# Kernel tuning notes

Measured on AMD Instinct MI355X. Metric: run time of the kernel, lower is better.

Reference implementation:

```python
import jax, jax.numpy as jnp
import numpy as np

N, E, IN, H, L, NB, G = 50000, 300000, 64, 256, 4, 181, 64
EPS = 1e-5
NEG_SLOPE = 0.2


def segment_softmax(e, seg, n):
    m = jax.ops.segment_max(e, seg, num_segments=n)
    a = jnp.exp(e - m[seg])
    d = jax.ops.segment_sum(a, seg, num_segments=n)
    return a / d[seg]


def setup_inputs() -> dict:
    key = jax.random.key(0)
    ks = jax.random.split(key, 32)
    p = lambda k, shape, fan: (jax.random.normal(k, shape, jnp.float32) / np.sqrt(fan)).astype(jnp.float32)
    inp = {}
    inp["x"] = jax.random.normal(ks[0], (N, IN), jnp.float32)
    inp["edge_index"] = jax.random.randint(ks[1], (2, E), 0, N, jnp.int64)
    inp["batch"] = jnp.sort(jax.random.randint(ks[2], (N,), 0, G, jnp.int64))
    inp["W_in"] = p(ks[3], (H, IN), IN); inp["b_in"] = jnp.zeros((H,), jnp.float32)
    inp["Wl"] = p(ks[4], (L, H, H), H); inp["bl"] = jnp.zeros((L, H), jnp.float32)
    inp["Wr"] = p(ks[5], (L, H, H), H); inp["br"] = jnp.zeros((L, H), jnp.float32)
    inp["att"] = p(ks[6], (L, H), H)
    inp["bias_c"] = jnp.zeros((L, H), jnp.float32)
    inp["ln_g"] = jnp.ones((L, H), jnp.float32); inp["ln_b"] = jnp.zeros((L, H), jnp.float32)
    inp["Wg1"] = p(ks[7], (H, H), H); inp["bg1"] = jnp.zeros((H,), jnp.float32)
    inp["Wg2"] = p(ks[8], (1, H), H); inp["bg2"] = jnp.zeros((1,), jnp.float32)
    inp["Ws"] = p(ks[9], (H, H), H); inp["bs"] = jnp.zeros((H,), jnp.float32)
    inp["Wc"] = p(ks[10], (NB, H), H); inp["bc"] = jnp.zeros((NB,), jnp.float32)
    inp["Wr1"] = p(ks[11], (128, H), H); inp["br1"] = jnp.zeros((128,), jnp.float32)
    inp["Wr2"] = p(ks[12], (1, 128), 128); inp["br2"] = jnp.zeros((1,), jnp.float32)
    return inp


def reference(x, edge_index, batch, W_in, b_in, Wl, bl, Wr, br, att, bias_c, ln_g, ln_b,
              Wg1, bg1, Wg2, bg2, Ws, bs, Wc, bc, Wr1, br1, Wr2, br2):
    n = x.shape[0]
    x = x @ W_in.T + b_in  # input projection -> [N,H]
    loops = jnp.arange(n)
    src = jnp.concatenate([edge_index[0], loops])  # GATv2 add_self_loops=True
    dst = jnp.concatenate([edge_index[1], loops])
    for l in range(L):
        x_res = x
        xl = x @ Wl[l].T + bl[l]  # lin_l (source)
        xr = x @ Wr[l].T + br[l]  # lin_r (target)
        h = jax.nn.leaky_relu(xl[src] + xr[dst], NEG_SLOPE)  # [E+N, H]
        e = h @ att[l]                                       # [E+N]
        alpha = segment_softmax(e, dst, n)
        out = jax.ops.segment_sum(alpha[:, None] * xl[src], dst, num_segments=n) + bias_c[l]
        mu = out.mean(-1, keepdims=True)
        var = out.var(-1, keepdims=True)
        out = (out - mu) / jnp.sqrt(var + EPS) * ln_g[l] + ln_b[l]
        x = jax.nn.relu(out) + x_res  # dropout is identity at eval
    gate = jax.nn.relu(x @ Wg1.T + bg1) @ Wg2.T + bg2  # [N,1]
    a = segment_softmax(gate[:, 0], batch, G)
    pooled = jax.ops.segment_sum(a[:, None] * x, batch, num_segments=G)  # [G,H]
    z = jax.nn.relu(pooled @ Ws.T + bs)
    cls_logits = z @ Wc.T + bc                                   # [G,NB]
    residual = jnp.tanh(jax.nn.relu(z @ Wr1.T + br1) @ Wr2.T + br2)[:, 0]  # [G]
    return cls_logits, residual
```

## Files before the change

kernel.cpp:

```cpp
#include <hip/hip_runtime.h>
#include <math.h>

#define N_NODES 50000
#define N_EDGES 300000
#define IN_DIM 64
#define H 256
#define LAYERS 4
#define NB 181
#define NGRAPH 64
#define EE (N_EDGES + N_NODES)
#define NEG_SLOPE 0.2f
#define LN_EPS 1e-5f

typedef unsigned short u16;
typedef __attribute__((ext_vector_type(8))) _Float16 half8;
typedef __attribute__((ext_vector_type(2))) _Float16 half2v;
typedef __attribute__((ext_vector_type(4))) float floatx4;

__device__ __forceinline__ u16 f2h(float f) {
  _Float16 h = (_Float16)f;
  return __builtin_bit_cast(u16, h);
}
__device__ __forceinline__ float h2f(u16 b) {
  return (float)__builtin_bit_cast(_Float16, b);
}

__device__ __forceinline__ float wave_reduce_sum(float v) {
  #pragma unroll
  for (int off = 32; off > 0; off >>= 1) v += __shfl_xor(v, off, 64);
  return v;
}

__global__ void cast_f16_kernel(const float* __restrict__ in, u16* __restrict__ out, int n4) {
  int i = blockIdx.x * 256 + threadIdx.x;
  if (i < n4) {
    float4 f = ((const float4*)in)[i];
    ushort4 o;
    o.x = f2h(f.x); o.y = f2h(f.y); o.z = f2h(f.z); o.w = f2h(f.w);
    ((ushort4*)out)[i] = o;
  }
}

__global__ void cast_weights_kernel(
    const float* __restrict__ W_in, const float* __restrict__ Wg1,
    const float* __restrict__ Wl, const float* __restrict__ Wr,
    u16* __restrict__ win_h, u16* __restrict__ wg1_h,
    u16* __restrict__ wl_h, u16* __restrict__ wr_h)
{
  int i = blockIdx.x * 256 + threadIdx.x;
  int which = blockIdx.y;
  const float* s; u16* dd; int n4;
  if (which == 0)      { s = W_in; dd = win_h; n4 = H * IN_DIM / 4; }
  else if (which == 1) { s = Wg1;  dd = wg1_h; n4 = H * H / 4; }
  else if (which == 2) { s = Wl;   dd = wl_h;  n4 = LAYERS * H * H / 4; }
  else                 { s = Wr;   dd = wr_h;  n4 = LAYERS * H * H / 4; }
  if (i < n4) {
    float4 f = ((const float4*)s)[i];
    ushort4 o;
    o.x = f2h(f.x); o.y = f2h(f.y); o.z = f2h(f.z); o.w = f2h(f.w);
    ((ushort4*)dd)[i] = o;
  }
}

__global__ void init_counts_kernel(int* __restrict__ cnt) {
  int i = blockIdx.x * 256 + threadIdx.x;
  if (i < N_NODES) cnt[i] = 1;
}

__global__ void count_edges_kernel(const int* __restrict__ dst, int* __restrict__ cnt) {
  int e = blockIdx.x * 256 + threadIdx.x;
  if (e < N_EDGES) atomicAdd(&cnt[dst[e]], 1);
}

__global__ void scan_blocks_kernel(const int* __restrict__ cnt, int* __restrict__ partial,
                                   int* __restrict__ bsums, int n) {
  __shared__ int buf[256];
  int tid = threadIdx.x;
  int i = blockIdx.x * 256 + tid;
  buf[tid] = (i < n) ? cnt[i] : 0;
  __syncthreads();
  #pragma unroll
  for (int off = 1; off < 256; off <<= 1) {
    int t = (tid >= off) ? buf[tid - off] : 0;
    __syncthreads();
    buf[tid] += t;
    __syncthreads();
  }
  if (i < n) partial[i] = buf[tid];
  if (tid == 255) bsums[blockIdx.x] = buf[255];
}

__global__ void scan_sums_kernel(int* __restrict__ bsums, int nblk) {
  __shared__ int buf[256];
  int tid = threadIdx.x;
  buf[tid] = (tid < nblk) ? bsums[tid] : 0;
  __syncthreads();
  #pragma unroll
  for (int off = 1; off < 256; off <<= 1) {
    int t = (tid >= off) ? buf[tid - off] : 0;
    __syncthreads();
    buf[tid] += t;
    __syncthreads();
  }
  if (tid < nblk) bsums[tid] = buf[tid];
}

__global__ void scan_write_kernel(const int* __restrict__ partial, const int* __restrict__ bsums,
                                  int* __restrict__ rowp, int n) {
  int i = blockIdx.x * 256 + threadIdx.x;
  if (i < n) {
    int b = blockIdx.x;
    int off = (b > 0) ? bsums[b - 1] : 0;
    rowp[i + 1] = partial[i] + off;
    if (i == 0) rowp[0] = 0;
  }
}

__global__ void fill_self_kernel(const int* __restrict__ rowp, int* __restrict__ col,
                                 int* __restrict__ fillpos) {
  int i = blockIdx.x * 256 + threadIdx.x;
  if (i < N_NODES) {
    int p = rowp[i];
    col[p] = i;
    fillpos[i] = p + 1;
  }
}

__global__ void fill_edges_kernel(const int* __restrict__ src, const int* __restrict__ dst,
                                  int* __restrict__ fillpos, int* __restrict__ col) {
  int e = blockIdx.x * 256 + threadIdx.x;
  if (e < N_EDGES) {
    int d = dst[e];
    int p = atomicAdd(&fillpos[d], 1);
    col[p] = src[e];
  }
}

#define GTM 128
#define GTK 64
#define LDB 72
#define SSTR 132

__global__ __launch_bounds__(256) void gemm_proj_kernel(
    const u16* __restrict__ A, const u16* __restrict__ W,
    const float* __restrict__ bias, u16* __restrict__ outh, int M, int K)
{
  __shared__ u16 smem[2 * GTM * LDB];
  u16* As = smem;
  u16* Bs = smem + GTM * LDB;
  int tid = threadIdx.x;
  int lane = tid & 63;
  int wave = tid >> 6;
  int wm = (wave >> 1) * 64;
  int wn = (wave & 1) * 64;
  int bm = blockIdx.y * GTM;
  int n0 = blockIdx.x * 128;
  int lr = tid >> 3;
  int lc = (tid & 7) * 8;

  floatx4 zero4 = {0.f, 0.f, 0.f, 0.f};
  floatx4 acc[4][4];
  #pragma unroll
  for (int i = 0; i < 4; i++)
    #pragma unroll
    for (int j = 0; j < 4; j++) acc[i][j] = zero4;

  int q8 = (lane >> 4) * 8;
  int mrow = lane & 15;

  for (int k0 = 0; k0 < K; k0 += GTK) {
    __syncthreads();
    #pragma unroll
    for (int p = 0; p < 4; p++) {
      int row = lr + p * 32;
      int gr = bm + row;
      uint4 av = {0, 0, 0, 0};
      if (gr < M) av = *(const uint4*)&A[(size_t)gr * K + k0 + lc];
      *(uint4*)&As[row * LDB + lc] = av;
      uint4 bv = *(const uint4*)&W[(size_t)(n0 + row) * K + k0 + lc];
      *(uint4*)&Bs[row * LDB + lc] = bv;
    }
    __syncthreads();
    #pragma unroll
    for (int h = 0; h < 2; h++) {
      half8 af[4], bf[4];
      #pragma unroll
      for (int i = 0; i < 4; i++)
        af[i] = *(const half8*)&As[(wm + i * 16 + mrow) * LDB + h * 32 + q8];
      #pragma unroll
      for (int j = 0; j < 4; j++)
        bf[j] = *(const half8*)&Bs[(wn + j * 16 + mrow) * LDB + h * 32 + q8];
      #pragma unroll
      for (int i = 0; i < 4; i++)
        #pragma unroll
        for (int j = 0; j < 4; j++)
          acc[i][j] = __builtin_amdgcn_mfma_f32_16x16x32_f16(af[i], bf[j], acc[i][j], 0, 0, 0);
    }
  }

  __syncthreads();
  u16* stage = smem;
  int ccol = lane & 15;
  int crow4 = (lane >> 4) * 4;
  #pragma unroll
  for (int j = 0; j < 4; j++) {
    float bv = bias[n0 + wn + j * 16 + ccol];
    #pragma unroll
    for (int i = 0; i < 4; i++) {
      #pragma unroll
      for (int r = 0; r < 4; r++) {
        int row = wm + i * 16 + crow4 + r;
        stage[row * SSTR + wn + j * 16 + ccol] = f2h(acc[i][j][r] + bv);
      }
    }
  }
  __syncthreads();
  int rr = tid >> 1;
  int c0 = (tid & 1) * 64;
  int grow = bm + rr;
  if (grow < M) {
    const ushort4* sp = (const ushort4*)&stage[rr * SSTR + c0];
    ushort4* gp = (ushort4*)&outh[(size_t)grow * H + n0 + c0];
    #pragma unroll
    for (int q = 0; q < 16; q++) gp[q] = sp[q];
  }
}

#define DTM 64
#define AST 264
#define SSTR2 132

__global__ __launch_bounds__(256) void gemm_dual2_kernel(
    const u16* __restrict__ A, const u16* __restrict__ Wlb, const u16* __restrict__ Wrb,
    const float* __restrict__ biasL, const float* __restrict__ biasR,
    u16* __restrict__ outL, u16* __restrict__ outR, int M)
{
  __shared__ u16 As[DTM * AST];
  __shared__ u16 Bs[128 * LDB];
  int tid = threadIdx.x;
  int lane = tid & 63;
  int wave = tid >> 6;
  int wn = wave * 32;
  int bm = blockIdx.x * DTM;
  int mrow = lane & 15;
  int q8 = (lane >> 4) * 8;
  int ccol = lane & 15;
  int crow4 = (lane >> 4) * 4;

  {
    int col = (tid & 31) * 8;
    int r0 = tid >> 5;
    #pragma unroll
    for (int it = 0; it < 8; it++) {
      int row = r0 + it * 8;
      int gr = bm + row;
      uint4 av = {0, 0, 0, 0};
      if (gr < M) av = *(const uint4*)&A[(size_t)gr * H + col];
      *(uint4*)&As[row * AST + col] = av;
    }
  }

  floatx4 zero4 = {0.f, 0.f, 0.f, 0.f};

  for (int nt = 0; nt < 4; nt++) {
    const u16* W = (nt < 2) ? Wlb : Wrb;
    const float* bias = (nt < 2) ? biasL : biasR;
    u16* outp = (nt < 2) ? outL : outR;
    int n0 = (nt & 1) * 128;

    floatx4 acc[4][2];
    #pragma unroll
    for (int i = 0; i < 4; i++) {
      acc[i][0] = zero4;
      acc[i][1] = zero4;
    }

    for (int k0 = 0; k0 < H; k0 += 64) {
      __syncthreads();
      {
        int col = (tid & 7) * 8;
        int r0 = tid >> 3;
        #pragma unroll
        for (int p2 = 0; p2 < 4; p2++) {
          int row = r0 + p2 * 32;
          uint4 bv = *(const uint4*)&W[(size_t)(n0 + row) * H + k0 + col];
          *(uint4*)&Bs[row * LDB + col] = bv;
        }
      }
      __syncthreads();
      #pragma unroll
      for (int h = 0; h < 2; h++) {
        half8 af[4], bf[2];
        #pragma unroll
        for (int i = 0; i < 4; i++)
          af[i] = *(const half8*)&As[(i * 16 + mrow) * AST + k0 + h * 32 + q8];
        #pragma unroll
        for (int j = 0; j < 2; j++)
          bf[j] = *(const half8*)&Bs[(wn + j * 16 + mrow) * LDB + h * 32 + q8];
        #pragma unroll
        for (int i = 0; i < 4; i++)
          #pragma unroll
          for (int j = 0; j < 2; j++)
            acc[i][j] = __builtin_amdgcn_mfma_f32_16x16x32_f16(af[i], bf[j], acc[i][j], 0, 0, 0);
      }
    }

    __syncthreads();
    u16* stage = Bs;
    #pragma unroll
    for (int j = 0; j < 2; j++) {
      float bv = bias[n0 + wn + j * 16 + ccol];
      #pragma unroll
      for (int i = 0; i < 4; i++) {
        #pragma unroll
        for (int r = 0; r < 4; r++) {
          int row = i * 16 + crow4 + r;
          stage[row * SSTR2 + wn + j * 16 + ccol] = f2h(acc[i][j][r] + bv);
        }
      }
    }
    __syncthreads();
    {
      int row = tid >> 2;
      int c0 = (tid & 3) * 32;
      int grow = bm + row;
      if (grow < M) {
        #pragma unroll
        for (int q = 0; q < 8; q++)
          *(ushort4*)&outp[(size_t)grow * H + n0 + c0 + q * 4] =
              *(const ushort4*)&stage[row * SSTR2 + c0 + q * 4];
      }
    }
  }
}

__global__ __launch_bounds__(256) void gemm_gate_kernel(
    const u16* __restrict__ A, const u16* __restrict__ W,
    const float* __restrict__ bias, const float* __restrict__ Wg2,
    float* __restrict__ gate, int M)
{
  __shared__ u16 smem[2 * GTM * LDB];
  u16* As = smem;
  u16* Bs = smem + GTM * LDB;
  int tid = threadIdx.x;
  int lane = tid & 63;
  int wave = tid >> 6;
  int wm = (wave >> 1) * 64;
  int wn = (wave & 1) * 64;
  int bm = blockIdx.y * GTM;
  int bn = blockIdx.x * 128;
  int lr = tid >> 3;
  int lc = (tid & 7) * 8;

  floatx4 zero4 = {0.f, 0.f, 0.f, 0.f};
  floatx4 acc[4][4];
  #pragma unroll
  for (int i = 0; i < 4; i++)
    #pragma unroll
    for (int j = 0; j < 4; j++) acc[i][j] = zero4;

  int q8 = (lane >> 4) * 8;
  int mrow = lane & 15;

  for (int k0 = 0; k0 < H; k0 += GTK) {
    __syncthreads();
    #pragma unroll
    for (int p = 0; p < 4; p++) {
      int row = lr + p * 32;
      int gr = bm + row;
      uint4 av = {0, 0, 0, 0};
      if (gr < M) av = *(const uint4*)&A[(size_t)gr * H + k0 + lc];
      *(uint4*)&As[row * LDB + lc] = av;
      uint4 bv = *(const uint4*)&W[(size_t)(bn + row) * H + k0 + lc];
      *(uint4*)&Bs[row * LDB + lc] = bv;
    }
    __syncthreads();
    #pragma unroll
    for (int h = 0; h < 2; h++) {
      half8 af[4], bf[4];
      #pragma unroll
      for (int i = 0; i < 4; i++)
        af[i] = *(const half8*)&As[(wm + i * 16 + mrow) * LDB + h * 32 + q8];
      #pragma unroll
      for (int j = 0; j < 4; j++)
        bf[j] = *(const half8*)&Bs[(wn + j * 16 + mrow) * LDB + h * 32 + q8];
      #pragma unroll
      for (int i = 0; i < 4; i++)
        #pragma unroll
        for (int j = 0; j < 4; j++)
          acc[i][j] = __builtin_amdgcn_mfma_f32_16x16x32_f16(af[i], bf[j], acc[i][j], 0, 0, 0);
    }
  }

  int ccol = lane & 15;
  float bv[4], wv[4];
  #pragma unroll
  for (int j = 0; j < 4; j++) {
    int col = bn + wn + j * 16 + ccol;
    bv[j] = bias[col];
    wv[j] = Wg2[col];
  }
  #pragma unroll
  for (int i = 0; i < 4; i++) {
    #pragma unroll
    for (int r = 0; r < 4; r++) {
      float p = 0.f;
      #pragma unroll
      for (int j = 0; j < 4; j++) {
        float hcol = fmaxf(acc[i][j][r] + bv[j], 0.f);
        p += hcol * wv[j];
      }
      p += __shfl_xor(p, 1, 64);
      p += __shfl_xor(p, 2, 64);
      p += __shfl_xor(p, 4, 64);
      p += __shfl_xor(p, 8, 64);
      int row = bm + wm + i * 16 + (lane >> 4) * 4 + r;
      if ((lane & 15) == 0 && row < M) atomicAdd(&gate[row], p);
    }
  }
}

__global__ __launch_bounds__(256) void layer_fused_kernel(
    const u16* __restrict__ xl, const u16* __restrict__ xr,
    u16* __restrict__ xst,
    const int* __restrict__ rowp, const int* __restrict__ col,
    const float* __restrict__ att, const float* __restrict__ bias_c,
    const float* __restrict__ ln_g, const float* __restrict__ ln_b)
{
  int lane = threadIdx.x & 63;
  int v = blockIdx.x * 4 + (threadIdx.x >> 6);
  if (v >= N_NODES) return;
  int slot = lane >> 5;
  int fl = lane & 31;
  int f8 = fl << 3;
  size_t rowbase = (size_t)v * H;

  uint4 xrq = *(const uint4*)&xr[rowbase + f8];
  half2v xrh[4] = {
    __builtin_bit_cast(half2v, xrq.x), __builtin_bit_cast(half2v, xrq.y),
    __builtin_bit_cast(half2v, xrq.z), __builtin_bit_cast(half2v, xrq.w)};
  float4 attA = *(const float4*)&att[f8];
  float4 attB = *(const float4*)&att[f8 + 4];
  half2v ath[4] = {
    {(_Float16)attA.x, (_Float16)attA.y}, {(_Float16)attA.z, (_Float16)attA.w},
    {(_Float16)attB.x, (_Float16)attB.y}, {(_Float16)attB.z, (_Float16)attB.w}};
  const half2v kslope = {(_Float16)NEG_SLOPE, (_Float16)NEG_SLOPE};

  int beg = rowp[v], end = rowp[v + 1];
  float m = -INFINITY, d = 0.f;
  float o[8] = {0.f, 0.f, 0.f, 0.f, 0.f, 0.f, 0.f, 0.f};

  for (int p = beg; p < end; p += 2) {
    int valid1 = (p + 1 < end);
    int u0 = col[p];
    int u1 = valid1 ? col[p + 1] : u0;
    int u = slot ? u1 : u0;
    uint4 aq = *(const uint4*)&xl[(size_t)u * H + f8];
    half2v ah[4] = {
      __builtin_bit_cast(half2v, aq.x), __builtin_bit_cast(half2v, aq.y),
      __builtin_bit_cast(half2v, aq.z), __builtin_bit_cast(half2v, aq.w)};
    float pe = 0.f;
    #pragma unroll
    for (int q = 0; q < 4; q++) {
      half2v h = ah[q] + xrh[q];
      half2v l = __builtin_elementwise_max(h, h * kslope);
#if __has_builtin(__builtin_amdgcn_fdot2)
      pe = __builtin_amdgcn_fdot2(l, ath[q], pe, false);
#else
      pe += (float)l[0] * (float)ath[q][0] + (float)l[1] * (float)ath[q][1];
#endif
    }
    #pragma unroll
    for (int off = 16; off > 0; off >>= 1) pe += __shfl_xor(pe, off, 64);
    if (slot && !valid1) pe = -INFINITY;
    float peO = __shfl_xor(pe, 32, 64);
    float mn = fmaxf(m, fmaxf(pe, peO));
    float sc = __expf(m - mn);
    float w = __expf(pe - mn);
    d = fmaf(d, sc, w);
    #pragma unroll
    for (int q = 0; q < 8; q++) {
      float af = (float)((q & 1) ? ah[q >> 1][1] : ah[q >> 1][0]);
      o[q] = fmaf(o[q], sc, w * af);
    }
    m = mn;
  }

  d += __shfl_xor(d, 32, 64);
  #pragma unroll
  for (int q = 0; q < 8; q++) o[q] += __shfl_xor(o[q], 32, 64);

  float invd = 1.0f / d;
  float4 bcA = *(const float4*)&bias_c[f8];
  float4 bcB = *(const float4*)&bias_c[f8 + 4];
  float bc[8] = {bcA.x, bcA.y, bcA.z, bcA.w, bcB.x, bcB.y, bcB.z, bcB.w};
  float ox[8];
  float part = 0.f;
  #pragma unroll
  for (int q = 0; q < 8; q++) {
    ox[q] = fmaf(o[q], invd, bc[q]);
    part += ox[q];
  }
  #pragma unroll
  for (int off = 16; off > 0; off >>= 1) part += __shfl_xor(part, off, 64);
  float mean = part * (1.0f / H);
  float sq = 0.f;
  #pragma unroll
  for (int q = 0; q < 8; q++) {
    ox[q] -= mean;
    sq = fmaf(ox[q], ox[q], sq);
  }
  #pragma unroll
  for (int off = 16; off > 0; off >>= 1) sq += __shfl_xor(sq, off, 64);
  float rstd = rsqrtf(sq * (1.0f / H) + LN_EPS);

  if (slot == 0) {
    float4 gA = *(const float4*)&ln_g[f8];
    float4 gB = *(const float4*)&ln_g[f8 + 4];
    float4 bA = *(const float4*)&ln_b[f8];
    float4 bB = *(const float4*)&ln_b[f8 + 4];
    float gg[8] = {gA.x, gA.y, gA.z, gA.w, gB.x, gB.y, gB.z, gB.w};
    float bb[8] = {bA.x, bA.y, bA.z, bA.w, bB.x, bB.y, bB.z, bB.w};
    uint4 resq = *(const uint4*)&xst[rowbase + f8];
    half2v rh[4] = {
      __builtin_bit_cast(half2v, resq.x), __builtin_bit_cast(half2v, resq.y),
      __builtin_bit_cast(half2v, resq.z), __builtin_bit_cast(half2v, resq.w)};
    u16 yout[8];
    #pragma unroll
    for (int q = 0; q < 8; q++) {
      float res = (float)((q & 1) ? rh[q >> 1][1] : rh[q >> 1][0]);
      float y = fmaxf(fmaf(ox[q] * rstd, gg[q], bb[q]), 0.f) + res;
      yout[q] = f2h(y);
    }
    *(uint4*)&xst[rowbase + f8] = *(const uint4*)yout;
  }
}

__global__ void gate_init_kernel(float* __restrict__ gate, const float* __restrict__ bg2,
                                 int* __restrict__ gstart, int* __restrict__ gend) {
  int i = blockIdx.x * 256 + threadIdx.x;
  if (i < N_NODES) gate[i] = bg2[0];
  if (i < NGRAPH) { gstart[i] = 0; gend[i] = 0; }
}

__global__ void gbounds_kernel(const int* __restrict__ batch, int* __restrict__ gstart,
                               int* __restrict__ gend) {
  int i = blockIdx.x * 256 + threadIdx.x;
  if (i < N_NODES) {
    int b = batch[i];
    if (i == 0 || batch[i - 1] != b) gstart[b] = i;
    if (i == N_NODES - 1 || batch[i + 1] != b) gend[b] = i + 1;
  }
}

__global__ __launch_bounds__(256) void pool_prep_kernel(
    const float* __restrict__ gate, const int* __restrict__ gstart,
    const int* __restrict__ gend, float* __restrict__ gmax, float* __restrict__ gdinv,
    float* __restrict__ pooled)
{
  __shared__ float red[256];
  int g = blockIdx.x, tid = threadIdx.x;
  pooled[(size_t)g * H + tid] = 0.f;
  int s = gstart[g], e = gend[g];
  float lm = -INFINITY;
  for (int i = s + tid; i < e; i += 256) lm = fmaxf(lm, gate[i]);
  red[tid] = lm;
  __syncthreads();
  for (int off = 128; off; off >>= 1) {
    if (tid < off) red[tid] = fmaxf(red[tid], red[tid + off]);
    __syncthreads();
  }
  float m = red[0];
  __syncthreads();
  float lsum = 0.0f;
  for (int i = s + tid; i < e; i += 256) lsum += __expf(gate[i] - m);
  red[tid] = lsum;
  __syncthreads();
  for (int off = 128; off; off >>= 1) {
    if (tid < off) red[tid] += red[tid + off];
    __syncthreads();
  }
  if (tid == 0) {
    gmax[g] = m;
    gdinv[g] = (s < e) ? 1.0f / red[0] : 0.0f;
  }
}

__global__ __launch_bounds__(256) void pool_accum_kernel(
    const float* __restrict__ gate, const u16* __restrict__ xh,
    const int* __restrict__ batch, const float* __restrict__ gmax,
    const float* __restrict__ gdinv, float* __restrict__ pooled)
{
  __shared__ float wl[128];
  __shared__ int gl[128];
  int b0 = blockIdx.x * 128;
  int tid = threadIdx.x;
  if (tid < 128) {
    int v = b0 + tid;
    if (v < N_NODES) {
      int g = batch[v];
      gl[tid] = g;
      wl[tid] = __expf(gate[v] - gmax[g]) * gdinv[g];
    } else {
      gl[tid] = -1;
      wl[tid] = 0.f;
    }
  }
  __syncthreads();
  int cnt = min(128, N_NODES - b0);
  float acc = 0.f;
  int cur = gl[0];
  for (int j = 0; j < cnt; j++) {
    int g = gl[j];
    if (g != cur) {
      atomicAdd(&pooled[(size_t)cur * H + tid], acc);
      acc = 0.f;
      cur = g;
    }
    acc += wl[j] * h2f(xh[(size_t)(b0 + j) * H + tid]);
  }
  if (cur >= 0) atomicAdd(&pooled[(size_t)cur * H + tid], acc);
}

__global__ __launch_bounds__(256) void head_kernel(
    const float* __restrict__ pooled,
    const float* __restrict__ Ws, const float* __restrict__ bs,
    const float* __restrict__ Wc, const float* __restrict__ bc,
    const float* __restrict__ Wr1, const float* __restrict__ br1,
    const float* __restrict__ Wr2, const float* __restrict__ br2,
    float* __restrict__ out)
{
  __shared__ float psh[256];
  __shared__ float zsh[256];
  __shared__ float r1sh[128];
  int g = blockIdx.x, tid = threadIdx.x;
  psh[tid] = pooled[(size_t)g * H + tid];
  __syncthreads();
  {
    float acc = bs[tid];
    const float4* wr = (const float4*)&Ws[(size_t)tid * H];
    for (int k4 = 0; k4 < H / 4; k4++) {
      float4 wv = wr[k4];
      float4 av = *(const float4*)&psh[k4 * 4];
      acc += av.x * wv.x + av.y * wv.y + av.z * wv.z + av.w * wv.w;
    }
    zsh[tid] = fmaxf(acc, 0.f);
  }
  __syncthreads();
  if (tid < NB) {
    float acc = bc[tid];
    const float4* wr = (const float4*)&Wc[(size_t)tid * H];
    for (int k4 = 0; k4 < H / 4; k4++) {
      float4 wv = wr[k4];
      float4 av = *(const float4*)&zsh[k4 * 4];
      acc += av.x * wv.x + av.y * wv.y + av.z * wv.z + av.w * wv.w;
    }
    out[(size_t)g * NB + tid] = acc;
  }
  if (tid < 128) {
    float acc = br1[tid];
    const float4* wr = (const float4*)&Wr1[(size_t)tid * H];
    for (int k4 = 0; k4 < H / 4; k4++) {
      float4 wv = wr[k4];
      float4 av = *(const float4*)&zsh[k4 * 4];
      acc += av.x * wv.x + av.y * wv.y + av.z * wv.z + av.w * wv.w;
    }
    r1sh[tid] = fmaxf(acc, 0.f);
  }
  __syncthreads();
  if (tid < 64) {
    float s2 = r1sh[tid] * Wr2[tid] + r1sh[tid + 64] * Wr2[tid + 64];
    s2 = wave_reduce_sum(s2);
    if (tid == 0) out[(size_t)NGRAPH * NB + g] = tanhf(s2 + br2[0]);
  }
}

extern "C" void kernel_launch(void* const* d_in, const int* in_sizes, int n_in,
                              void* d_out, int out_size, void* d_ws, size_t ws_size,
                              hipStream_t stream) {
  const float* x_in   = (const float*)d_in[0];
  const int*   eidx   = (const int*)d_in[1];
  const int*   batch  = (const int*)d_in[2];
  const float* W_in   = (const float*)d_in[3];
  const float* b_in   = (const float*)d_in[4];
  const float* Wl     = (const float*)d_in[5];
  const float* bl     = (const float*)d_in[6];
  const float* Wr     = (const float*)d_in[7];
  const float* br     = (const float*)d_in[8];
  const float* att    = (const float*)d_in[9];
  const float* bias_c = (const float*)d_in[10];
  const float* ln_g   = (const float*)d_in[11];
  const float* ln_b   = (const float*)d_in[12];
  const float* Wg1    = (const float*)d_in[13];
  const float* bg1    = (const float*)d_in[14];
  const float* Wg2    = (const float*)d_in[15];
  const float* bg2    = (const float*)d_in[16];
  const float* Ws     = (const float*)d_in[17];
  const float* bs     = (const float*)d_in[18];
  const float* Wc     = (const float*)d_in[19];
  const float* bc     = (const float*)d_in[20];
  const float* Wr1    = (const float*)d_in[21];
  const float* br1    = (const float*)d_in[22];
  const float* Wr2    = (const float*)d_in[23];
  const float* br2    = (const float*)d_in[24];
  float* out = (float*)d_out;

  char* w = (char*)d_ws;
  u16* x_h    = (u16*)w;    w += sizeof(u16) * (size_t)N_NODES * H;
  u16* xl_h   = (u16*)w;    w += sizeof(u16) * (size_t)N_NODES * H;
  u16* xr_h   = (u16*)w;    w += sizeof(u16) * (size_t)N_NODES * H;
  u16* xin_h  = (u16*)w;    w += sizeof(u16) * (size_t)N_NODES * IN_DIM;
  u16* win_h  = (u16*)w;    w += sizeof(u16) * (size_t)H * IN_DIM;
  u16* wl_h   = (u16*)w;    w += sizeof(u16) * (size_t)LAYERS * H * H;
  u16* wr_h   = (u16*)w;    w += sizeof(u16) * (size_t)LAYERS * H * H;
  u16* wg1_h  = (u16*)w;    w += sizeof(u16) * (size_t)H * H;
  float* pooled = (float*)w; w += sizeof(float) * NGRAPH * H;
  float* gate = (float*)w;  w += sizeof(float) * N_NODES;
  float* gmax = (float*)w;  w += sizeof(float) * NGRAPH;
  float* gdinv= (float*)w;  w += sizeof(float) * NGRAPH;
  int* cnt    = (int*)w;    w += sizeof(int) * N_NODES;
  int* rowp   = (int*)w;    w += sizeof(int) * (N_NODES + 1);
  int* col    = (int*)w;    w += sizeof(int) * EE;
  int* partial= (int*)w;    w += sizeof(int) * N_NODES;
  int* bsums  = (int*)w;    w += sizeof(int) * 256;
  int* gstart = (int*)w;    w += sizeof(int) * NGRAPH;
  int* gend   = (int*)w;    w += sizeof(int) * NGRAPH;
  (void)ws_size; (void)n_in; (void)in_sizes; (void)out_size;

  const int* src = eidx;
  const int* dst = eidx + N_EDGES;
  int nblkN = (N_NODES + 255) / 256;
  int nblkE = (N_EDGES + 255) / 256;
  int mtiles = (N_NODES + GTM - 1) / GTM;
  int mtiles2 = (N_NODES + DTM - 1) / DTM;

  init_counts_kernel<<<nblkN, 256, 0, stream>>>(cnt);
  count_edges_kernel<<<nblkE, 256, 0, stream>>>(dst, cnt);
  scan_blocks_kernel<<<nblkN, 256, 0, stream>>>(cnt, partial, bsums, N_NODES);
  scan_sums_kernel<<<1, 256, 0, stream>>>(bsums, nblkN);
  scan_write_kernel<<<nblkN, 256, 0, stream>>>(partial, bsums, rowp, N_NODES);
  fill_self_kernel<<<nblkN, 256, 0, stream>>>(rowp, col, cnt);
  fill_edges_kernel<<<nblkE, 256, 0, stream>>>(src, dst, cnt, col);

  {
    int maxn4 = LAYERS * H * H / 4;
    dim3 gcast((maxn4 + 255) / 256, 4);
    cast_weights_kernel<<<gcast, 256, 0, stream>>>(W_in, Wg1, Wl, Wr,
                                                   win_h, wg1_h, wl_h, wr_h);
    int n4 = N_NODES * IN_DIM / 4;
    cast_f16_kernel<<<(n4 + 255) / 256, 256, 0, stream>>>(x_in, xin_h, n4);
  }

  dim3 gproj(2, mtiles);
  gemm_proj_kernel<<<gproj, 256, 0, stream>>>(xin_h, win_h, b_in, x_h, N_NODES, IN_DIM);

  int nblkV = N_NODES / 4;
  for (int l = 0; l < LAYERS; l++) {
    gemm_dual2_kernel<<<mtiles2, 256, 0, stream>>>(x_h,
        wl_h + (size_t)l * H * H, wr_h + (size_t)l * H * H,
        bl + l * H, br + l * H, xl_h, xr_h, N_NODES);
    layer_fused_kernel<<<nblkV, 256, 0, stream>>>(xl_h, xr_h, x_h, rowp, col,
        att + l * H, bias_c + l * H, ln_g + l * H, ln_b + l * H);
  }

  gate_init_kernel<<<nblkN, 256, 0, stream>>>(gate, bg2, gstart, gend);
  dim3 ggate(2, mtiles);
  gemm_gate_kernel<<<ggate, 256, 0, stream>>>(x_h, wg1_h, bg1, Wg2, gate, N_NODES);

  gbounds_kernel<<<nblkN, 256, 0, stream>>>(batch, gstart, gend);
  pool_prep_kernel<<<NGRAPH, 256, 0, stream>>>(gate, gstart, gend, gmax, gdinv, pooled);
  pool_accum_kernel<<<(N_NODES + 127) / 128, 256, 0, stream>>>(gate, x_h, batch, gmax, gdinv, pooled);

  head_kernel<<<NGRAPH, 256, 0, stream>>>(pooled, Ws, bs, Wc, bc, Wr1, br1, Wr2, br2, out);
}
```

Measured before the change: 653.3 us.

## Remap GAT aggregation so each lane owns 4 features and accumulates in fp16

The per-node attention aggregation kernel previously split the wave into two 32-lane halves, each handling one neighbour with 8 features per lane. It now has all 64 lanes cover the full 256-feature row at 4 features per lane and load both neighbours per iteration. This removes the cross-half shuffles and the idle half-wave in the LayerNorm epilogue, but each iteration now needs a 64-wide reduction for two scores. The output accumulator is also switched from fp32 to packed fp16 FMA, which lowers register use and instruction count at the cost of accumulation precision.

```diff
diff --git a/kernel.cpp b/kernel.cpp
--- a/kernel.cpp
+++ b/kernel.cpp
@@ -430,110 +430,91 @@
   int lane = threadIdx.x & 63;
   int v = blockIdx.x * 4 + (threadIdx.x >> 6);
   if (v >= N_NODES) return;
-  int slot = lane >> 5;
-  int fl = lane & 31;
-  int f8 = fl << 3;
+  int f4 = lane << 2;
   size_t rowbase = (size_t)v * H;
 
-  uint4 xrq = *(const uint4*)&xr[rowbase + f8];
-  half2v xrh[4] = {
-    __builtin_bit_cast(half2v, xrq.x), __builtin_bit_cast(half2v, xrq.y),
-    __builtin_bit_cast(half2v, xrq.z), __builtin_bit_cast(half2v, xrq.w)};
-  float4 attA = *(const float4*)&att[f8];
-  float4 attB = *(const float4*)&att[f8 + 4];
-  half2v ath[4] = {
-    {(_Float16)attA.x, (_Float16)attA.y}, {(_Float16)attA.z, (_Float16)attA.w},
-    {(_Float16)attB.x, (_Float16)attB.y}, {(_Float16)attB.z, (_Float16)attB.w}};
+  uint2 xrq = *(const uint2*)&xr[rowbase + f4];
+  half2v xrh[2] = {__builtin_bit_cast(half2v, xrq.x), __builtin_bit_cast(half2v, xrq.y)};
+  float4 attv = *(const float4*)&att[f4];
+  half2v ath[2] = {{(_Float16)attv.x, (_Float16)attv.y},
+                   {(_Float16)attv.z, (_Float16)attv.w}};
   const half2v kslope = {(_Float16)NEG_SLOPE, (_Float16)NEG_SLOPE};
 
   int beg = rowp[v], end = rowp[v + 1];
   float m = -INFINITY, d = 0.f;
-  float o[8] = {0.f, 0.f, 0.f, 0.f, 0.f, 0.f, 0.f, 0.f};
+  half2v o0 = {(_Float16)0.f, (_Float16)0.f};
+  half2v o1 = {(_Float16)0.f, (_Float16)0.f};
 
   for (int p = beg; p < end; p += 2) {
     int valid1 = (p + 1 < end);
     int u0 = col[p];
     int u1 = valid1 ? col[p + 1] : u0;
-    int u = slot ? u1 : u0;
-    uint4 aq = *(const uint4*)&xl[(size_t)u * H + f8];
-    half2v ah[4] = {
-      __builtin_bit_cast(half2v, aq.x), __builtin_bit_cast(half2v, aq.y),
-      __builtin_bit_cast(half2v, aq.z), __builtin_bit_cast(half2v, aq.w)};
-    float pe = 0.f;
-    #pragma unroll
-    for (int q = 0; q < 4; q++) {
-      half2v h = ah[q] + xrh[q];
-      half2v l = __builtin_elementwise_max(h, h * kslope);
+    uint2 aq0 = *(const uint2*)&xl[(size_t)u0 * H + f4];
+    uint2 aq1 = *(const uint2*)&xl[(size_t)u1 * H + f4];
+    half2v a00 = __builtin_bit_cast(half2v, aq0.x);
+    half2v a01 = __builtin_bit_cast(half2v, aq0.y);
+    half2v a10 = __builtin_bit_cast(half2v, aq1.x);
+    half2v a11 = __builtin_bit_cast(half2v, aq1.y);
+    half2v h00 = a00 + xrh[0], h01 = a01 + xrh[1];
+    half2v h10 = a10 + xrh[0], h11 = a11 + xrh[1];
+    half2v l00 = __builtin_elementwise_max(h00, h00 * kslope);
+    half2v l01 = __builtin_elementwise_max(h01, h01 * kslope);
+    half2v l10 = __builtin_elementwise_max(h10, h10 * kslope);
+    half2v l11 = __builtin_elementwise_max(h11, h11 * kslope);
 #if __has_builtin(__builtin_amdgcn_fdot2)
-      pe = __builtin_amdgcn_fdot2(l, ath[q], pe, false);
+    float pe0 = __builtin_amdgcn_fdot2(l01, ath[1],
+                 __builtin_amdgcn_fdot2(l00, ath[0], 0.f, false), false);
+    float pe1 = __builtin_amdgcn_fdot2(l11, ath[1],
+                 __builtin_amdgcn_fdot2(l10, ath[0], 0.f, false), false);
 #else
-      pe += (float)l[0] * (float)ath[q][0] + (float)l[1] * (float)ath[q][1];
+    float pe0 = (float)l00[0] * (float)ath[0][0] + (float)l00[1] * (float)ath[0][1]
+              + (float)l01[0] * (float)ath[1][0] + (float)l01[1] * (float)ath[1][1];
+    float pe1 = (float)l10[0] * (float)ath[0][0] + (float)l10[1] * (float)ath[0][1]
+              + (float)l11[0] * (float)ath[1][0] + (float)l11[1] * (float)ath[1][1];
 #endif
-    }
-    #pragma unroll
-    for (int off = 16; off > 0; off >>= 1) pe += __shfl_xor(pe, off, 64);
-    if (slot && !valid1) pe = -INFINITY;
-    float peO = __shfl_xor(pe, 32, 64);
-    float mn = fmaxf(m, fmaxf(pe, peO));
+    #pragma unroll
+    for (int off = 32; off > 0; off >>= 1) {
+      pe0 += __shfl_xor(pe0, off, 64);
+      pe1 += __shfl_xor(pe1, off, 64);
+    }
+    if (!valid1) pe1 = -INFINITY;
+    float mn = fmaxf(m, fmaxf(pe0, pe1));
     float sc = __expf(m - mn);
-    float w = __expf(pe - mn);
-    d = fmaf(d, sc, w);
-    #pragma unroll
-    for (int q = 0; q < 8; q++) {
-      float af = (float)((q & 1) ? ah[q >> 1][1] : ah[q >> 1][0]);
-      o[q] = fmaf(o[q], sc, w * af);
-    }
+    float w0 = __expf(pe0 - mn);
+    float w1 = __expf(pe1 - mn);
+    d = fmaf(d, sc, w0 + w1);
+    _Float16 sch = (_Float16)sc, w0h = (_Float16)w0, w1h = (_Float16)w1;
+    half2v scp = {sch, sch}, w0p = {w0h, w0h}, w1p = {w1h, w1h};
+    half2v t0 = a00 * w0p + a10 * w1p;
+    half2v t1 = a01 * w0p + a11 * w1p;
+    o0 = o0 * scp + t0;
+    o1 = o1 * scp + t1;
     m = mn;
   }
 
-  d += __shfl_xor(d, 32, 64);
-  #pragma unroll
-  for (int q = 0; q < 8; q++) o[q] += __shfl_xor(o[q], 32, 64);
-
   float invd = 1.0f / d;
-  float4 bcA = *(const float4*)&bias_c[f8];
-  float4 bcB = *(const float4*)&bias_c[f8 + 4];
-  float bc[8] = {bcA.x, bcA.y, bcA.z, bcA.w, bcB.x, bcB.y, bcB.z, bcB.w};
-  float ox[8];
-  float part = 0.f;
-  #pragma unroll
-  for (int q = 0; q < 8; q++) {
-    ox[q] = fmaf(o[q], invd, bc[q]);
-    part += ox[q];
-  }
-  #pragma unroll
-  for (int off = 16; off > 0; off >>= 1) part += __shfl_xor(part, off, 64);
-  float mean = part * (1.0f / H);
-  float sq = 0.f;
-  #pragma unroll
-  for (int q = 0; q < 8; q++) {
-    ox[q] -= mean;
-    sq = fmaf(ox[q], ox[q], sq);
-  }
-  #pragma unroll
-  for (int off = 16; off > 0; off >>= 1) sq += __shfl_xor(sq, off, 64);
+  float4 bc4 = *(const float4*)&bias_c[f4];
+  float ox = fmaf((float)o0[0], invd, bc4.x);
+  float oy = fmaf((float)o0[1], invd, bc4.y);
+  float oz = fmaf((float)o1[0], invd, bc4.z);
+  float ow = fmaf((float)o1[1], invd, bc4.w);
+  float s = wave_reduce_sum(ox + oy + oz + ow);
+  float mean = s * (1.0f / H);
+  float cx = ox - mean, cy = oy - mean, cz = oz - mean, cw = ow - mean;
+  float sq = wave_reduce_sum(cx * cx + cy * cy + cz * cz + cw * cw);
   float rstd = rsqrtf(sq * (1.0f / H) + LN_EPS);
-
-  if (slot == 0) {
-    float4 gA = *(const float4*)&ln_g[f8];
-    float4 gB = *(const float4*)&ln_g[f8 + 4];
-    float4 bA = *(const float4*)&ln_b[f8];
-    float4 bB = *(const float4*)&ln_b[f8 + 4];
-    float gg[8] = {gA.x, gA.y, gA.z, gA.w, gB.x, gB.y, gB.z, gB.w};
-    float bb[8] = {bA.x, bA.y, bA.z, bA.w, bB.x, bB.y, bB.z, bB.w};
-    uint4 resq = *(const uint4*)&xst[rowbase + f8];
-    half2v rh[4] = {
-      __builtin_bit_cast(half2v, resq.x), __builtin_bit_cast(half2v, resq.y),
-      __builtin_bit_cast(half2v, resq.z), __builtin_bit_cast(half2v, resq.w)};
-    u16 yout[8];
-    #pragma unroll
-    for (int q = 0; q < 8; q++) {
-      float res = (float)((q & 1) ? rh[q >> 1][1] : rh[q >> 1][0]);
-      float y = fmaxf(fmaf(ox[q] * rstd, gg[q], bb[q]), 0.f) + res;
-      yout[q] = f2h(y);
-    }
-    *(uint4*)&xst[rowbase + f8] = *(const uint4*)yout;
-  }
+  float4 g4 = *(const float4*)&ln_g[f4];
+  float4 b4 = *(const float4*)&ln_b[f4];
+  uint2 resq = *(const uint2*)&xst[rowbase + f4];
+  half2v r0 = __builtin_bit_cast(half2v, resq.x);
+  half2v r1 = __builtin_bit_cast(half2v, resq.y);
+  float yx = fmaxf(fmaf(cx * rstd, g4.x, b4.x), 0.f) + (float)r0[0];
+  float yy = fmaxf(fmaf(cy * rstd, g4.y, b4.y), 0.f) + (float)r0[1];
+  float yz = fmaxf(fmaf(cz * rstd, g4.z, b4.z), 0.f) + (float)r1[0];
+  float yw = fmaxf(fmaf(cw * rstd, g4.w, b4.w), 0.f) + (float)r1[1];
+  ushort4 yb;
+  yb.x = f2h(yx); yb.y = f2h(yy); yb.z = f2h(yz); yb.w = f2h(yw);
+  *(ushort4*)&xst[rowbase + f4] = yb;
 }
 
 __global__ void gate_init_kernel(float* __restrict__ gate, const float* __restrict__ bg2,
```

After: 651.1 us. About the same (-0.3%).
